# Optimization experiments

Hardware: AMD Instinct MI355X
Metric: run time of the kernel (lower is better)

The kernel has to match this reference:

```python
import jax, jax.numpy as jnp
import numpy as np

B, S, D = 4, 2048, 1024


def setup_inputs() -> dict:
    key = jax.random.key(0)
    k1, k2 = jax.random.split(key)
    x = jax.random.normal(k1, (B, S, D), dtype=jnp.float32)
    W_qkv = jax.random.normal(k2, (D, 3 * D), dtype=jnp.float32) * 0.02
    # causal mask: 1 where attendable, 0 where masked (broadcast over batch)
    attention_mask = jnp.tril(jnp.ones((S, S), dtype=jnp.int32))[None, :, :]
    return {"input": x, "W_qkv": W_qkv, "attention_mask": attention_mask}


def reference(input, W_qkv, attention_mask):
    # fused QKV projection (nn.Linear, bias=False)
    qkv = jnp.einsum('bsd,de->bse', input, W_qkv)  # [B, S, 3D]
    q, k, v = jnp.split(qkv, 3, axis=-1)           # each [B, S, D]
    scale = 1.0 / jnp.sqrt(jnp.asarray(D, dtype=input.dtype))
    scores = jnp.einsum('bqd,bkd->bqk', q, k) * scale  # [B, S, S]
    neg_inf = jnp.finfo(scores.dtype).min
    scores = jnp.where(attention_mask == 0, neg_inf, scores)
    attn = jax.nn.softmax(scores, axis=-1)
    # dropout prob = 0.0 -> identity
    out = jnp.einsum('bqk,bkd->bqd', attn, v)      # [B, S, D]
    return out
```

## Files before the change

kernel.cpp:

```cpp
#include <hip/hip_runtime.h>
#include <hip/hip_bf16.h>


typedef __attribute__((ext_vector_type(8))) short short8;
typedef __attribute__((ext_vector_type(4))) short s16x4;
typedef __attribute__((ext_vector_type(4))) float f32x4;
typedef __attribute__((ext_vector_type(16))) float f32x16;

__device__ __forceinline__ short f2bf(float f) {
  __hip_bfloat16 h = __float2bfloat16(f);
  return *reinterpret_cast<short*>(&h);
}

__device__ __forceinline__ void gll16(const void* g, void* l) {
  __builtin_amdgcn_global_load_lds((const __attribute__((address_space(1))) void*)g,
                                   (__attribute__((address_space(3))) void*)l,
                                   16, 0, 0);
}

__device__ __forceinline__ void ntst_f(float* p, float v) { __builtin_nontemporal_store(v, p); }

__device__ __forceinline__ void gemm_core3232(const short* __restrict__ A,
                                              const short* __restrict__ Bt,
                                              int lda, int ldb,
                                              int row0, int col0, int kIters,
                                              f32x16 acc[2][2],
                                              short* lA, short* lB) {
  const int tid  = threadIdx.x;
  const int wave = tid >> 6;
  const int lane = tid & 63;
  const int l32  = lane & 31;
  const int hi   = lane >> 5;

#pragma unroll
  for (int i = 0; i < 2; ++i)
#pragma unroll
    for (int j = 0; j < 2; ++j)
#pragma unroll
      for (int e = 0; e < 16; ++e) acc[i][j][e] = 0.f;

  const int srow = tid >> 3;
  const int gcol = ((tid & 7) ^ (srow & 7)) * 8;
  const short* A1 = A + (size_t)(row0 + srow) * lda + gcol;
  const short* A2 = A + (size_t)(row0 + srow + 32) * lda + gcol;
  const short* A3 = A + (size_t)(row0 + srow + 64) * lda + gcol;
  const short* A4 = A + (size_t)(row0 + srow + 96) * lda + gcol;
  const short* B1 = Bt + (size_t)(col0 + srow) * ldb + gcol;
  const short* B2 = Bt + (size_t)(col0 + srow + 32) * ldb + gcol;
  const short* B3 = Bt + (size_t)(col0 + srow + 64) * ldb + gcol;
  const short* B4 = Bt + (size_t)(col0 + srow + 96) * ldb + gcol;

  short* lA1 = lA + wave * 512;
  short* lA2 = lA + 2048 + wave * 512;
  short* lA3 = lA + 4096 + wave * 512;
  short* lA4 = lA + 6144 + wave * 512;
  short* lB1 = lB + wave * 512;
  short* lB2 = lB + 2048 + wave * 512;
  short* lB3 = lB + 4096 + wave * 512;
  short* lB4 = lB + 6144 + wave * 512;

  const int rb = (wave >> 1) * 64;
  const int cb = (wave & 1) * 64;
  const short* aBase = lA + (rb + l32) * 64;
  const short* bBase = lB + (cb + l32) * 64;
  const int swz = l32 & 7;

  for (int it = 0; it < kIters; ++it) {
    const int k0 = it * 64;
    gll16(A1 + k0, lA1);
    gll16(A2 + k0, lA2);
    gll16(A3 + k0, lA3);
    gll16(A4 + k0, lA4);
    gll16(B1 + k0, lB1);
    gll16(B2 + k0, lB2);
    gll16(B3 + k0, lB3);
    gll16(B4 + k0, lB4);
    __syncthreads();

#pragma unroll
    for (int ks = 0; ks < 4; ++ks) {
      const int kss = (ks + wave) & 3;
      const int so = ((kss * 2 + hi) ^ swz) * 8;
      short8 a0 = *(const short8*)(aBase + so);
      short8 a1 = *(const short8*)(aBase + 2048 + so);
      short8 b0 = *(const short8*)(bBase + so);
      short8 b1 = *(const short8*)(bBase + 2048 + so);
      acc[0][0] = __builtin_amdgcn_mfma_f32_32x32x16_bf16(a0, b0, acc[0][0], 0, 0, 0);
      acc[0][1] = __builtin_amdgcn_mfma_f32_32x32x16_bf16(a0, b1, acc[0][1], 0, 0, 0);
      acc[1][0] = __builtin_amdgcn_mfma_f32_32x32x16_bf16(a1, b0, acc[1][0], 0, 0, 0);
      acc[1][1] = __builtin_amdgcn_mfma_f32_32x32x16_bf16(a1, b1, acc[1][1], 0, 0, 0);
    }
    __syncthreads();
  }
}

__device__ __forceinline__ void gemm_core64(const short* __restrict__ A,
                                            const short* __restrict__ Bt,
                                            int lda, int ldb,
                                            int row0, int col0, int kIters,
                                            f32x4 acc[4][2],
                                            short* lA, short* lB) {
  const int tid  = threadIdx.x;
  const int wave = tid >> 6;
  const int lane = tid & 63;
  const int quad = lane >> 4;
  const int l16  = lane & 15;

  const f32x4 zero = {0.f, 0.f, 0.f, 0.f};
#pragma unroll
  for (int i = 0; i < 4; ++i)
#pragma unroll
    for (int j = 0; j < 2; ++j) acc[i][j] = zero;

  const int srow = tid >> 3;
  const int gcol = ((tid & 7) ^ (srow & 7)) * 8;
  const short* A1 = A + (size_t)(row0 + srow) * lda + gcol;
  const short* A2 = A + (size_t)(row0 + srow + 32) * lda + gcol;
  const short* B1 = Bt + (size_t)(col0 + srow) * ldb + gcol;
  const short* B2 = Bt + (size_t)(col0 + srow + 32) * ldb + gcol;
  const short* B3 = Bt + (size_t)(col0 + srow + 64) * ldb + gcol;
  const short* B4 = Bt + (size_t)(col0 + srow + 96) * ldb + gcol;

  short* lA1 = lA + wave * 512;
  short* lA2 = lA + 2048 + wave * 512;
  short* lB1 = lB + wave * 512;
  short* lB2 = lB + 2048 + wave * 512;
  short* lB3 = lB + 4096 + wave * 512;
  short* lB4 = lB + 6144 + wave * 512;

  const int rswz  = l16 & 7;
  const int slot0 = (quad ^ rswz) * 8;
  const int slot1 = ((4 + quad) ^ rswz) * 8;
  const short* aRow = lA + l16 * 64;
  const short* bRow = lB + (wave * 32 + l16) * 64;

  for (int it = 0; it < kIters; ++it) {
    const int k0 = it * 64;
    gll16(A1 + k0, lA1);
    gll16(A2 + k0, lA2);
    gll16(B1 + k0, lB1);
    gll16(B2 + k0, lB2);
    gll16(B3 + k0, lB3);
    gll16(B4 + k0, lB4);
    __syncthreads();

#pragma unroll
    for (int s = 0; s < 2; ++s) {
      const int so = s ? slot1 : slot0;
      short8 af[4], bfr[2];
#pragma unroll
      for (int i = 0; i < 4; ++i) af[i] = *(const short8*)(aRow + i * 1024 + so);
#pragma unroll
      for (int j = 0; j < 2; ++j) bfr[j] = *(const short8*)(bRow + j * 1024 + so);
#pragma unroll
      for (int i = 0; i < 4; ++i)
#pragma unroll
        for (int j = 0; j < 2; ++j)
          acc[i][j] = __builtin_amdgcn_mfma_f32_16x16x32_bf16(af[i], bfr[j], acc[i][j], 0, 0, 0);
    }
    __syncthreads();
  }
}

__global__ __launch_bounds__(256) void setup_kernel(const float* __restrict__ X,
                                                    const float* __restrict__ W,
                                                    short* __restrict__ Xb,
                                                    short* __restrict__ Wt,
                                                    float* __restrict__ rs) {
  const int bid = blockIdx.x;
  if (bid < 8192) {
    const int i = (bid * 256 + threadIdx.x) * 4;
    const f32x4 v = *(const f32x4*)(X + i);
    s16x4 o;
    o.x = f2bf(v.x); o.y = f2bf(v.y); o.z = f2bf(v.z); o.w = f2bf(v.w);
    *(s16x4*)(Xb + i) = o;
  } else if (bid < 11264) {
    __shared__ float tile[32][33];
    const int r  = bid - 8192;
    const int ni = r % 96;
    const int ki = r / 96;
    const int tx = threadIdx.x & 31;
    const int ty = threadIdx.x >> 5;
#pragma unroll
    for (int rr = 0; rr < 4; ++rr)
      tile[ty + rr * 8][tx] = W[(size_t)(ki * 32 + ty + rr * 8) * 3072 + ni * 32 + tx];
    __syncthreads();
#pragma unroll
    for (int rr = 0; rr < 4; ++rr)
      Wt[(size_t)(ni * 32 + ty + rr * 8) * 1024 + ki * 32 + tx] = f2bf(tile[tx][ty + rr * 8]);
  } else {
    const int i = (bid - 11264) * 1024 + threadIdx.x * 4;
    const f32x4 zero = {0.f, 0.f, 0.f, 0.f};
    *(f32x4*)(rs + i) = zero;
  }
}

__global__ __launch_bounds__(256) void qkv_gemm_kernel(const short* __restrict__ Xb,
                                                       const short* __restrict__ Wt,
                                                       short* __restrict__ Q,
                                                       short* __restrict__ K,
                                                       short* __restrict__ Vt) {
  __shared__ short lA[8192], lB[8192];
  const int br = blockIdx.x / 24;
  const int bc = blockIdx.x % 24;
  f32x16 acc[2][2];
  gemm_core3232(Xb, Wt, 1024, 1024, br * 128, bc * 128, 16, acc, lA, lB);

  const int lane = threadIdx.x & 63;
  const int wave = threadIdx.x >> 6;
  const int l32  = lane & 31;
  const int hi   = lane >> 5;
  const int rbase = br * 128 + (wave >> 1) * 64;
  const int cbase = bc * 128 + (wave & 1) * 64;

  if (bc < 16) {
#pragma unroll
    for (int fi = 0; fi < 2; ++fi)
#pragma unroll
      for (int fj = 0; fj < 2; ++fj) {
        const int col = cbase + fj * 32 + l32;
        short* dst = (col < 1024) ? Q : K;
        const int n = col & 1023;
#pragma unroll
        for (int reg = 0; reg < 16; ++reg) {
          const int row = rbase + fi * 32 + (reg & 3) + 8 * (reg >> 2) + 4 * hi;
          dst[(size_t)row * 1024 + n] = f2bf(acc[fi][fj][reg]);
        }
      }
  } else {
    const int b  = rbase >> 11;
    const int s0 = rbase & 2047;
    short* VtB = Vt + (size_t)b * 1024 * 2048;
#pragma unroll
    for (int fi = 0; fi < 2; ++fi)
#pragma unroll
      for (int fj = 0; fj < 2; ++fj) {
        const int d = cbase - 2048 + fj * 32 + l32;
#pragma unroll
        for (int g = 0; g < 4; ++g) {
          const int sb = s0 + fi * 32 + 8 * g + 4 * hi;
          s16x4 pk;
          pk.x = f2bf(acc[fi][fj][4 * g + 0]);
          pk.y = f2bf(acc[fi][fj][4 * g + 1]);
          pk.z = f2bf(acc[fi][fj][4 * g + 2]);
          pk.w = f2bf(acc[fi][fj][4 * g + 3]);
          *(s16x4*)(VtB + (size_t)d * 2048 + sb) = pk;
        }
      }
  }
}

__global__ __launch_bounds__(256) void qk_kernel(const short* __restrict__ Q,
                                                 const short* __restrict__ K,
                                                 short* __restrict__ E,
                                                 float* __restrict__ rs) {
  __shared__ short lA[4096], lB[8192];
  const int orig = blockIdx.x;
  const int g = (orig & 7) * 136 + (orig >> 3);
  const int t = g >> 2;
  const int b = g & 3;
  int qi = 31, off = t;
  while (off >= (qi >> 1) + 1) { off -= (qi >> 1) + 1; qi--; }
  const int ki = off;

  f32x4 acc[4][2];
  const short* Qb = Q + (size_t)b * 2048 * 1024;
  const short* Kb = K + (size_t)b * 2048 * 1024;
  gemm_core64(Qb, Kb, 1024, 1024, qi * 64, ki * 128, 16, acc, lA, lB);

  const int lane = threadIdx.x & 63;
  const int wave = threadIdx.x >> 6;
  const int quad = lane >> 4;
  const int l16  = lane & 15;
  short* Eb  = E + (size_t)b * 2048 * 2048;
  float* rsb = rs + b * 2048;
  const int rbase = qi * 64;
  const int cbase = ki * 128 + wave * 32;
  const bool diag = (ki == (qi >> 1));
#pragma unroll
  for (int i = 0; i < 4; ++i)
#pragma unroll
    for (int r = 0; r < 4; ++r) {
      const int row = rbase + i * 16 + quad * 4 + r;
      float partial = 0.f;
#pragma unroll
      for (int j = 0; j < 2; ++j) {
        const int col = cbase + j * 16 + l16;
        float e = __expf(acc[i][j][r] * 0.03125f);
        if (diag && col > row) e = 0.f;
        partial += e;
        Eb[(size_t)row * 2048 + col] = f2bf(e);
      }
      partial += __shfl_xor(partial, 1);
      partial += __shfl_xor(partial, 2);
      partial += __shfl_xor(partial, 4);
      partial += __shfl_xor(partial, 8);
      if (l16 == 0) atomicAdd(rsb + row, partial);
    }
}

__global__ __launch_bounds__(256) void pv_kernel(const short* __restrict__ E,
                                                 const short* __restrict__ Vt,
                                                 const float* __restrict__ rs,
                                                 float* __restrict__ out) {
  __shared__ short lA[4096], lB[8192];
  const int orig = blockIdx.x;
  const int g = (orig & 7) * 128 + (orig >> 3);
  const int t   = g >> 2;
  const int b   = g & 3;
  const int qi  = 31 - (t >> 3);
  const int dj  = t & 7;

  f32x4 acc[4][2];
  const short* Eb  = E + (size_t)b * 2048 * 2048;
  const short* Vtb = Vt + (size_t)b * 1024 * 2048;
  gemm_core64(Eb, Vtb, 2048, 2048, qi * 64, dj * 128, qi + 1, acc, lA, lB);

  const int lane = threadIdx.x & 63;
  const int wave = threadIdx.x >> 6;
  const int quad = lane >> 4;
  const int l16  = lane & 15;
  float* ob = out + (size_t)b * 2048 * 1024;
  const float* rsb = rs + b * 2048;
  const int rbase = qi * 64;
  const int cbase = dj * 128 + wave * 32;
#pragma unroll
  for (int i = 0; i < 4; ++i)
#pragma unroll
    for (int r2 = 0; r2 < 4; ++r2) {
      const int row = rbase + i * 16 + quad * 4 + r2;
      const float inv = 1.f / rsb[row];
#pragma unroll
      for (int j = 0; j < 2; ++j) {
        const int col = cbase + j * 16 + l16;
        ntst_f(&ob[(size_t)row * 1024 + col], acc[i][j][r2] * inv);
      }
    }
}

extern "C" void kernel_launch(void* const* d_in, const int* in_sizes, int n_in,
                              void* d_out, int out_size, void* d_ws, size_t ws_size,
                              hipStream_t stream) {
  const float* X = (const float*)d_in[0];
  const float* W = (const float*)d_in[1];
  float* out = (float*)d_out;
  char* w = (char*)d_ws;

  short* Xb = (short*)(w + 0);
  short* Wt = (short*)(w + 16777216);
  short* E  = (short*)(w + 0);
  float* rs = (float*)(w + 50331648);
  short* Q  = (short*)(w + 67108864);
  short* K  = (short*)(w + 83886080);
  short* Vt = (short*)(w + 100663296);

  hipLaunchKernelGGL(setup_kernel,    dim3(11272), dim3(256), 0, stream, X, W, Xb, Wt, rs);
  hipLaunchKernelGGL(qkv_gemm_kernel, dim3(1536),  dim3(256), 0, stream, Xb, Wt, Q, K, Vt);
  hipLaunchKernelGGL(qk_kernel,       dim3(1088),  dim3(256), 0, stream, Q, K, E, rs);
  hipLaunchKernelGGL(pv_kernel,       dim3(1024),  dim3(256), 0, stream, E, Vt, rs, out);
}
```

Measured before the change: 245.7 us.

## Merge QK and PV kernels into one persistent kernel with grid barrier

Fuses the QK-exp kernel and the PV kernel into a single launch separated by a software grid-wide barrier (an atomic counter reset in the setup kernel). This removes one kernel launch and the inter-kernel drain/ramp gap. The barrier needs all 1088 blocks to be co-resident, which launch_bounds(256,5) is meant to allow on 256 CUs. If they cannot all be resident the kernel deadlocks. Blocks that finish QK early also sit idle spinning at the barrier.

```diff
diff --git a/kernel.cpp b/kernel.cpp
--- a/kernel.cpp
+++ b/kernel.cpp
@@ -6,6 +6,8 @@
 typedef __attribute__((ext_vector_type(4))) short s16x4;
 typedef __attribute__((ext_vector_type(4))) float f32x4;
 typedef __attribute__((ext_vector_type(16))) float f32x16;
+
+#define ATTN_BLOCKS 1088u
 
 __device__ __forceinline__ short f2bf(float f) {
   __hip_bfloat16 h = __float2bfloat16(f);
@@ -166,7 +168,8 @@
                                                     const float* __restrict__ W,
                                                     short* __restrict__ Xb,
                                                     short* __restrict__ Wt,
-                                                    float* __restrict__ rs) {
+                                                    float* __restrict__ rs,
+                                                    unsigned int* __restrict__ bar) {
   const int bid = blockIdx.x;
   if (bid < 8192) {
     const int i = (bid * 256 + threadIdx.x) * 4;
@@ -188,10 +191,12 @@
 #pragma unroll
     for (int rr = 0; rr < 4; ++rr)
       Wt[(size_t)(ni * 32 + ty + rr * 8) * 1024 + ki * 32 + tx] = f2bf(tile[tx][ty + rr * 8]);
-  } else {
+  } else if (bid < 11272) {
     const int i = (bid - 11264) * 1024 + threadIdx.x * 4;
     const f32x4 zero = {0.f, 0.f, 0.f, 0.f};
     *(f32x4*)(rs + i) = zero;
+  } else {
+    if (threadIdx.x == 0) *bar = 0u;
   }
 }
 
@@ -250,92 +255,103 @@
   }
 }
 
-__global__ __launch_bounds__(256) void qk_kernel(const short* __restrict__ Q,
-                                                 const short* __restrict__ K,
-                                                 short* __restrict__ E,
-                                                 float* __restrict__ rs) {
+__global__ __launch_bounds__(256, 5) void attn_kernel(const short* __restrict__ Q,
+                                                      const short* __restrict__ K,
+                                                      const short* __restrict__ Vt,
+                                                      short* __restrict__ E,
+                                                      float* __restrict__ rs,
+                                                      float* __restrict__ out,
+                                                      unsigned int* __restrict__ bar) {
   __shared__ short lA[4096], lB[8192];
-  const int orig = blockIdx.x;
-  const int g = (orig & 7) * 136 + (orig >> 3);
-  const int t = g >> 2;
-  const int b = g & 3;
-  int qi = 31, off = t;
-  while (off >= (qi >> 1) + 1) { off -= (qi >> 1) + 1; qi--; }
-  const int ki = off;
-
-  f32x4 acc[4][2];
-  const short* Qb = Q + (size_t)b * 2048 * 1024;
-  const short* Kb = K + (size_t)b * 2048 * 1024;
-  gemm_core64(Qb, Kb, 1024, 1024, qi * 64, ki * 128, 16, acc, lA, lB);
-
-  const int lane = threadIdx.x & 63;
-  const int wave = threadIdx.x >> 6;
-  const int quad = lane >> 4;
-  const int l16  = lane & 15;
-  short* Eb  = E + (size_t)b * 2048 * 2048;
-  float* rsb = rs + b * 2048;
-  const int rbase = qi * 64;
-  const int cbase = ki * 128 + wave * 32;
-  const bool diag = (ki == (qi >> 1));
-#pragma unroll
-  for (int i = 0; i < 4; ++i)
-#pragma unroll
-    for (int r = 0; r < 4; ++r) {
-      const int row = rbase + i * 16 + quad * 4 + r;
-      float partial = 0.f;
-#pragma unroll
-      for (int j = 0; j < 2; ++j) {
-        const int col = cbase + j * 16 + l16;
-        float e = __expf(acc[i][j][r] * 0.03125f);
-        if (diag && col > row) e = 0.f;
-        partial += e;
-        Eb[(size_t)row * 2048 + col] = f2bf(e);
+
+  {
+    const int orig = blockIdx.x;
+    const int g = (orig & 7) * 136 + (orig >> 3);
+    const int t = g >> 2;
+    const int b = g & 3;
+    int qi = 31, off = t;
+    while (off >= (qi >> 1) + 1) { off -= (qi >> 1) + 1; qi--; }
+    const int ki = off;
+
+    f32x4 acc[4][2];
+    const short* Qb = Q + (size_t)b * 2048 * 1024;
+    const short* Kb = K + (size_t)b * 2048 * 1024;
+    gemm_core64(Qb, Kb, 1024, 1024, qi * 64, ki * 128, 16, acc, lA, lB);
+
+    const int lane = threadIdx.x & 63;
+    const int wave = threadIdx.x >> 6;
+    const int quad = lane >> 4;
+    const int l16  = lane & 15;
+    short* Eb  = E + (size_t)b * 2048 * 2048;
+    float* rsb = rs + b * 2048;
+    const int rbase = qi * 64;
+    const int cbase = ki * 128 + wave * 32;
+    const bool diag = (ki == (qi >> 1));
+#pragma unroll
+    for (int i = 0; i < 4; ++i)
+#pragma unroll
+      for (int r = 0; r < 4; ++r) {
+        const int row = rbase + i * 16 + quad * 4 + r;
+        float partial = 0.f;
+#pragma unroll
+        for (int j = 0; j < 2; ++j) {
+          const int col = cbase + j * 16 + l16;
+          float e = __expf(acc[i][j][r] * 0.03125f);
+          if (diag && col > row) e = 0.f;
+          partial += e;
+          Eb[(size_t)row * 2048 + col] = f2bf(e);
+        }
+        partial += __shfl_xor(partial, 1);
+        partial += __shfl_xor(partial, 2);
+        partial += __shfl_xor(partial, 4);
+        partial += __shfl_xor(partial, 8);
+        if (l16 == 0) atomicAdd(rsb + row, partial);
       }
-      partial += __shfl_xor(partial, 1);
-      partial += __shfl_xor(partial, 2);
-      partial += __shfl_xor(partial, 4);
-      partial += __shfl_xor(partial, 8);
-      if (l16 == 0) atomicAdd(rsb + row, partial);
-    }
-}
-
-__global__ __launch_bounds__(256) void pv_kernel(const short* __restrict__ E,
-                                                 const short* __restrict__ Vt,
-                                                 const float* __restrict__ rs,
-                                                 float* __restrict__ out) {
-  __shared__ short lA[4096], lB[8192];
-  const int orig = blockIdx.x;
-  const int g = (orig & 7) * 128 + (orig >> 3);
-  const int t   = g >> 2;
-  const int b   = g & 3;
-  const int qi  = 31 - (t >> 3);
-  const int dj  = t & 7;
-
-  f32x4 acc[4][2];
-  const short* Eb  = E + (size_t)b * 2048 * 2048;
-  const short* Vtb = Vt + (size_t)b * 1024 * 2048;
-  gemm_core64(Eb, Vtb, 2048, 2048, qi * 64, dj * 128, qi + 1, acc, lA, lB);
-
-  const int lane = threadIdx.x & 63;
-  const int wave = threadIdx.x >> 6;
-  const int quad = lane >> 4;
-  const int l16  = lane & 15;
-  float* ob = out + (size_t)b * 2048 * 1024;
-  const float* rsb = rs + b * 2048;
-  const int rbase = qi * 64;
-  const int cbase = dj * 128 + wave * 32;
-#pragma unroll
-  for (int i = 0; i < 4; ++i)
-#pragma unroll
-    for (int r2 = 0; r2 < 4; ++r2) {
-      const int row = rbase + i * 16 + quad * 4 + r2;
-      const float inv = 1.f / rsb[row];
-#pragma unroll
-      for (int j = 0; j < 2; ++j) {
-        const int col = cbase + j * 16 + l16;
-        ntst_f(&ob[(size_t)row * 1024 + col], acc[i][j][r2] * inv);
+  }
+
+  __syncthreads();
+  if (threadIdx.x == 0) {
+    __hip_atomic_fetch_add(bar, 1u, __ATOMIC_RELEASE, __HIP_MEMORY_SCOPE_AGENT);
+    while (__hip_atomic_load(bar, __ATOMIC_ACQUIRE, __HIP_MEMORY_SCOPE_AGENT) < ATTN_BLOCKS)
+      __builtin_amdgcn_s_sleep(16);
+  }
+  __syncthreads();
+  __threadfence();
+
+  if (blockIdx.x < 1024) {
+    const int orig = blockIdx.x;
+    const int g = (orig & 7) * 128 + (orig >> 3);
+    const int t   = g >> 2;
+    const int b   = g & 3;
+    const int qi  = 31 - (t >> 3);
+    const int dj  = t & 7;
+
+    f32x4 acc[4][2];
+    const short* Eb  = E + (size_t)b * 2048 * 2048;
+    const short* Vtb = Vt + (size_t)b * 1024 * 2048;
+    gemm_core64(Eb, Vtb, 2048, 2048, qi * 64, dj * 128, qi + 1, acc, lA, lB);
+
+    const int lane = threadIdx.x & 63;
+    const int wave = threadIdx.x >> 6;
+    const int quad = lane >> 4;
+    const int l16  = lane & 15;
+    float* ob = out + (size_t)b * 2048 * 1024;
+    const float* rsb = rs + b * 2048;
+    const int rbase = qi * 64;
+    const int cbase = dj * 128 + wave * 32;
+#pragma unroll
+    for (int i = 0; i < 4; ++i)
+#pragma unroll
+      for (int r2 = 0; r2 < 4; ++r2) {
+        const int row = rbase + i * 16 + quad * 4 + r2;
+        const float inv = 1.f / rsb[row];
+#pragma unroll
+        for (int j = 0; j < 2; ++j) {
+          const int col = cbase + j * 16 + l16;
+          ntst_f(&ob[(size_t)row * 1024 + col], acc[i][j][r2] * inv);
+        }
       }
-    }
+  }
 }
 
 extern "C" void kernel_launch(void* const* d_in, const int* in_sizes, int n_in,
@@ -350,12 +366,12 @@
   short* Wt = (short*)(w + 16777216);
   short* E  = (short*)(w + 0);
   float* rs = (float*)(w + 50331648);
+  unsigned int* bar = (unsigned int*)(w + 50364416);
   short* Q  = (short*)(w + 67108864);
   short* K  = (short*)(w + 83886080);
   short* Vt = (short*)(w + 100663296);
 
-  hipLaunchKernelGGL(setup_kernel,    dim3(11272), dim3(256), 0, stream, X, W, Xb, Wt, rs);
+  hipLaunchKernelGGL(setup_kernel,    dim3(11273), dim3(256), 0, stream, X, W, Xb, Wt, rs, bar);
   hipLaunchKernelGGL(qkv_gemm_kernel, dim3(1536),  dim3(256), 0, stream, Xb, Wt, Q, K, Vt);
-  hipLaunchKernelGGL(qk_kernel,       dim3(1088),  dim3(256), 0, stream, Q, K, E, rs);
-  hipLaunchKernelGGL(pv_kernel,       dim3(1024),  dim3(256), 0, stream, E, Vt, rs, out);
-}
+  hipLaunchKernelGGL(attn_kernel,     dim3(1088),  dim3(256), 0, stream, Q, K, Vt, E, rs, out, bar);
+}
```

Measured after the change: 534.9 us. 2.18x slower.
